# Optimization experiments

Hardware: AMD Instinct MI355X
Metric: run time of the kernel (lower is better)

## Reference

```python
import jax, jax.numpy as jnp
import numpy as np

B, S, T, E, H, Vt, Vs, M = 16, 64, 64, 256, 512, 32000, 32000, 100
J = 2 * M + 1


def _lstm(x, lengths, Wx, Wh, b, reverse=False):
    # TF LSTMCell (forget_bias=1.0) with sequence_length masking, optional reverse_sequence.
    Bn, Tn, _ = x.shape
    Hn = Wh.shape[0]
    tpos = jnp.arange(Tn)
    ridx = None
    if reverse:
        ridx = jnp.where(tpos[None, :] < lengths[:, None], lengths[:, None] - 1 - tpos[None, :], tpos[None, :])
        x = jnp.take_along_axis(x, ridx[:, :, None], axis=1)
    mask = (tpos[:, None] < lengths[None, :])[:, :, None]  # [T,B,1]
    xT = jnp.swapaxes(x, 0, 1)  # [T,B,E]

    def step(carry, inp):
        h, c = carry
        xt, mt = inp
        g = xt @ Wx + h @ Wh + b
        i, j, f, o = jnp.split(g, 4, axis=-1)
        c_new = jax.nn.sigmoid(f + 1.0) * c + jax.nn.sigmoid(i) * jnp.tanh(j)
        h_new = jax.nn.sigmoid(o) * jnp.tanh(c_new)
        c2 = jnp.where(mt, c_new, c)
        h2 = jnp.where(mt, h_new, h)
        return (h2, c2), jnp.where(mt, h_new, jnp.zeros_like(h_new))

    init = (jnp.zeros((Bn, Hn), x.dtype), jnp.zeros((Bn, Hn), x.dtype))
    _, ys = jax.lax.scan(step, init, (xT, mask))
    ys = jnp.swapaxes(ys, 0, 1)  # [B,T,H]
    if reverse:
        ys = jnp.take_along_axis(ys, ridx[:, :, None], axis=1)
    return ys


def setup_inputs() -> dict:
    key = jax.random.key(0)
    ks = jax.random.split(key, 24)
    sc = 0.05
    n = lambda k, shape: (jax.random.normal(k, shape, jnp.float32) * sc)
    inp = {
        "sources": jax.random.randint(ks[0], (B, S), 0, Vs, jnp.int32),
        "targets": jax.random.randint(ks[1], (B, T), 0, Vt, jnp.int32),
        "targets_null": jnp.array([Vt - 1], jnp.int32),
        "target_lengths": jax.random.randint(ks[2], (B,), T // 2, T + 1, jnp.int32),
        "emb": n(ks[3], (Vt, E)),
        "nnW": n(ks[4], (E, H)),
        "nnb": jnp.zeros((H,), jnp.float32),
        "Wx_fw": n(ks[5], (E, 4 * H)),
        "Wh_fw": n(ks[6], (H, 4 * H)),
        "b_fw": jnp.zeros((4 * H,), jnp.float32),
        "Wx_bw": n(ks[7], (E, 4 * H)),
        "Wh_bw": n(ks[8], (H, 4 * H)),
        "b_bw": jnp.zeros((4 * H,), jnp.float32),
        "Wproj_e": n(ks[9], (2 * H, H)),
        "Wv": n(ks[10], (H, Vs)),
        "bv": jnp.zeros((Vs,), jnp.float32),
        "Wproj_t": n(ks[11], (2 * H, E)),
        "Wj": n(ks[12], (H, J)),
        "bj": jnp.zeros((J,), jnp.float32),
        "Wp0": n(ks[13], (H, 1)),
        "bp0": jnp.zeros((1,), jnp.float32),
    }
    return inp


def reference(sources, targets, targets_null, target_lengths, emb, nnW, nnb,
              Wx_fw, Wh_fw, b_fw, Wx_bw, Wh_bw, b_bw, Wproj_e, Wv, bv,
              Wproj_t, Wj, bj, Wp0, bp0):
    x = emb[targets]                              # [B,T,E]
    x_null = emb[targets_null]                    # [1,E]
    null_state = jnp.tanh(x_null @ nnW + nnb)     # [1,H]
    h_fw = _lstm(x, target_lengths, Wx_fw, Wh_fw, b_fw, False)
    h_bw = _lstm(x, target_lengths, Wx_bw, Wh_bw, b_bw, True)
    h_cat = jnp.concatenate([h_fw, h_bw], axis=-1)  # [B,T,2H]

    # ---- emission ----
    ts = h_cat @ Wproj_e                          # [B,T,H]
    probs = jax.nn.softmax(ts @ Wv + bv, axis=-1)             # [B,T,Vs]
    null_probs = jax.nn.softmax(null_state @ Wv + bv, axis=-1)  # [1,Vs]
    e_word = jnp.take_along_axis(probs, sources[:, None, :].astype(jnp.int32), axis=2)  # [B,T,S]
    e_null = jnp.broadcast_to(null_probs[0][sources][:, None, :], e_word.shape)
    emission = jnp.concatenate([e_word, e_null], axis=1)       # [B,2T,S]

    # ---- transition ----
    tt = jnp.tanh((h_cat @ Wproj_t) @ nnW + nnb)  # [B,T,H]
    jump = jax.nn.softmax(tt @ Wj + bj, axis=-1)  # [B,T,J]
    p0 = jax.nn.sigmoid(tt @ Wp0 + bp0)[..., 0]   # [B,T]
    Tn = targets.shape[1]
    # entry (i,j) <- jump[i, M + j - i] (the tf.map_fn gather over word_idx)
    idx = M + jnp.arange(Tn)[None, :] - jnp.arange(Tn)[:, None]  # [T,T]
    jw = jnp.take_along_axis(jump, jnp.broadcast_to(idx[None], (jump.shape[0], Tn, Tn)), axis=2)  # [B,T,T]
    eye = jnp.eye(Tn, dtype=jw.dtype)
    half = jnp.concatenate([jw, p0[:, :, None] * eye], axis=2)            # [B,T,2T]
    transition = jnp.concatenate([half, half], axis=1)                    # [B,2T,2T]
    lhalf = jnp.concatenate([jnp.log(jw), jnp.log(p0)[:, :, None] * eye], axis=2)
    transition_log = jnp.concatenate([lhalf, lhalf], axis=1)
    return emission, transition, transition_log
```

## Files before the change

### kernel.cpp

```cpp
#include <hip/hip_runtime.h>
#include <hip/hip_bf16.h>
#include <math.h>

#define Bn 16
#define Sn 64
#define Tn 64
#define En 256
#define Hn 512
#define VS 32000
#define Jn 201
#define Mn 100

#define O_HCATF  0
#define O_DENOM  524288
#define O_NULLD  525312
#define O_SLOTS  525376
#define O_HBUF   527424
#define ZERO_N   560192
#define O_NS     560192
#define O_TS     560704
#define O_TSF    1084992
#define O_TTPRE  1347136
#define O_TTPF   1609280
#define O_TT     1740352
#define O_XF     2264640
#define O_WVC    2264640
#define O_WXFW   2395712
#define O_WXBW   2657856
#define O_WPEF   2920000
#define O_WPTF   3182144
#define O_NNWF   3313216
#define O_GX     3378752

typedef __attribute__((ext_vector_type(8))) short short8;
typedef __attribute__((ext_vector_type(4))) float f32x4;

__device__ __forceinline__ float sigf(float x) { return 1.0f / (1.0f + expf(-x)); }
__device__ __forceinline__ unsigned short tobf(float x) {
    __hip_bfloat16 h = __float2bfloat16(x);
    return *reinterpret_cast<unsigned short*>(&h);
}

__device__ __forceinline__ void dconvA(const float* __restrict__ A, uint4* __restrict__ out,
                                       int K, const int* __restrict__ gidx, int g) {
    int Kd = K >> 5;
    int lane = g & 63, t = g >> 6;
    int ks = t % Kd, mt = t / Kd;
    int m = mt * 16 + (lane & 15);
    int k0 = ks * 32 + (lane >> 4) * 8;
    const float* p = (gidx ? A + (size_t)gidx[m] * K : A + (size_t)m * K) + k0;
    float4 f0 = *(const float4*)(p);
    float4 f1 = *(const float4*)(p + 4);
    unsigned short u[8] = {tobf(f0.x), tobf(f0.y), tobf(f0.z), tobf(f0.w),
                           tobf(f1.x), tobf(f1.y), tobf(f1.z), tobf(f1.w)};
    out[g] = *(uint4*)u;
}

__device__ __forceinline__ void dconvB(const float* __restrict__ B, uint4* __restrict__ out,
                                       int N, int K, int g) {
    int Kd = K >> 5;
    int lane = g & 63, t = g >> 6;
    int ks = t % Kd, nt = t / Kd;
    int n = nt * 16 + (lane & 15);
    int k0 = ks * 32 + (lane >> 4) * 8;
    const float* p = B + (size_t)k0 * N + n;
    unsigned short u[8];
#pragma unroll
    for (int j = 0; j < 8; j++) u[j] = tobf(p[(size_t)j * N]);
    out[g] = *(uint4*)u;
}

__global__ __launch_bounds__(256) void convA2_k(const float* __restrict__ ttpre,
                                                uint4* __restrict__ ttpf,
                                                const float* __restrict__ ts,
                                                uint4* __restrict__ tsf) {
    int blk = blockIdx.x, tid = threadIdx.x;
    if (blk < 128) dconvA(ttpre, ttpf, 256, nullptr, blk * 256 + tid);
    else           dconvA(ts, tsf, 512, nullptr, (blk - 128) * 256 + tid);
}

__global__ __launch_bounds__(256) void mega_prep_k(float4* __restrict__ zdst, int zn4,
                                                   const float* __restrict__ emb,
                                                   const int* __restrict__ targets,
                                                   uint4* __restrict__ xf,
                                                   const float* __restrict__ wxfw, uint4* __restrict__ wxfwf,
                                                   const float* __restrict__ wxbw, uint4* __restrict__ wxbwf) {
    int blk = blockIdx.x, tid = threadIdx.x;
    if (blk < 548) {
        int i = blk * 256 + tid;
        if (i < zn4) zdst[i] = make_float4(0.f, 0.f, 0.f, 0.f);
    } else if (blk < 676) {
        dconvA(emb, xf, 256, targets, (blk - 548) * 256 + tid);
    } else if (blk < 932) {
        dconvB(wxfw, wxfwf, 2048, 256, (blk - 676) * 256 + tid);
    } else {
        dconvB(wxbw, wxbwf, 2048, 256, (blk - 932) * 256 + tid);
    }
}

template <int ACT>
__device__ __forceinline__ void gemm_body(const uint4* __restrict__ af,
                                          const uint4* __restrict__ bf,
                                          const float* __restrict__ bias,
                                          float* __restrict__ C, int N, int Kd,
                                          int bx, int by) {
    int tid = threadIdx.x, w = tid >> 6, lane = tid & 63;
    int ntb = bx * 8 + w * 2;
    int mtb = by * 8;
    f32x4 acc[8][2];
#pragma unroll
    for (int i = 0; i < 8; i++)
#pragma unroll
        for (int j = 0; j < 2; j++) acc[i][j] = 0.0f;
    for (int ks = 0; ks < Kd; ++ks) {
        uint4 b0 = bf[(size_t)(ntb * Kd + ks) * 64 + lane];
        uint4 b1 = bf[(size_t)((ntb + 1) * Kd + ks) * 64 + lane];
#pragma unroll
        for (int i = 0; i < 8; i++) {
            uint4 a = af[(size_t)((mtb + i) * Kd + ks) * 64 + lane];
            acc[i][0] = __builtin_amdgcn_mfma_f32_16x16x32_bf16(
                *reinterpret_cast<short8*>(&a), *reinterpret_cast<short8*>(&b0), acc[i][0], 0, 0, 0);
            acc[i][1] = __builtin_amdgcn_mfma_f32_16x16x32_bf16(
                *reinterpret_cast<short8*>(&a), *reinterpret_cast<short8*>(&b1), acc[i][1], 0, 0, 0);
        }
    }
    int n0 = ntb * 16 + (lane & 15);
    int q = lane >> 4;
    float bs0 = bias ? bias[n0] : 0.f;
    float bs1 = bias ? bias[n0 + 16] : 0.f;
#pragma unroll
    for (int i = 0; i < 8; i++)
#pragma unroll
        for (int r = 0; r < 4; r++) {
            int m = (mtb + i) * 16 + q * 4 + r;
            float v0 = acc[i][0][r] + bs0;
            float v1 = acc[i][1][r] + bs1;
            if (ACT == 1) { v0 = tanhf(v0); v1 = tanhf(v1); }
            C[(size_t)m * N + n0] = v0;
            C[(size_t)m * N + n0 + 16] = v1;
        }
}

template <int ACT>
__global__ __launch_bounds__(256) void gemm_mfma_k(const uint4* __restrict__ af,
                                                   const uint4* __restrict__ bf,
                                                   const float* __restrict__ bias,
                                                   float* __restrict__ C, int N, int Kd) {
    gemm_body<ACT>(af, bf, bias, C, N, Kd, blockIdx.x, blockIdx.y);
}

__global__ __launch_bounds__(256) void gx_gemm_k(const uint4* __restrict__ xf,
                                                 const uint4* __restrict__ wxfwf,
                                                 const uint4* __restrict__ wxbwf,
                                                 const float* __restrict__ b_fw,
                                                 const float* __restrict__ b_bw,
                                                 float* __restrict__ gx) {
    int bx = blockIdx.x;
    if (bx < 16) gemm_body<0>(xf, wxfwf, b_fw, gx, 2048, 8, bx, blockIdx.y);
    else         gemm_body<0>(xf, wxbwf, b_bw, gx + 2097152, 2048, 8, bx - 16, blockIdx.y);
}

__global__ __launch_bounds__(256) void proj_gemm_k(const uint4* __restrict__ hcatf,
                                                   const uint4* __restrict__ wpef,
                                                   const uint4* __restrict__ wptf,
                                                   float* __restrict__ ts,
                                                   float* __restrict__ ttpre) {
    int bx = blockIdx.x;
    if (bx < 4) gemm_body<0>(hcatf, wpef, nullptr, ts, 512, 32, bx, blockIdx.y);
    else        gemm_body<0>(hcatf, wptf, nullptr, ttpre, 256, 32, bx - 4, blockIdx.y);
}

__global__ __launch_bounds__(256, 1) void lstm_fused_k(const float* __restrict__ wh_fw,
                                                       const float* __restrict__ wh_bw,
                                                       const float* __restrict__ gx,
                                                       const int* __restrict__ lengths,
                                                       unsigned* __restrict__ hbuf32,
                                                       unsigned* __restrict__ hcat32,
                                                       unsigned* __restrict__ slots,
                                                       const float* __restrict__ Wv,
                                                       const float* __restrict__ emb,
                                                       const int* __restrict__ tnull,
                                                       const float* __restrict__ nnW,
                                                       const float* __restrict__ nnb,
                                                       const float* __restrict__ bv,
                                                       float* __restrict__ ns,
                                                       float* __restrict__ nd,
                                                       const int* __restrict__ sources,
                                                       float* __restrict__ wvc,
                                                       const float* __restrict__ wpe, uint4* __restrict__ wpef,
                                                       const float* __restrict__ wpt, uint4* __restrict__ wptf,
                                                       const float* __restrict__ nnw2, uint4* __restrict__ nnwf) {
    int blk = blockIdx.x;
    int tid = threadIdx.x;

    if (blk >= 669) {
        dconvB(nnw2, nnwf, 512, 256, (blk - 669) * 256 + tid);
        return;
    }
    if (blk >= 541) {
        dconvB(wpt, wptf, 256, 1024, (blk - 541) * 256 + tid);
        return;
    }
    if (blk >= 285) {
        dconvB(wpe, wpef, 512, 1024, (blk - 285) * 256 + tid);
        return;
    }
    if (blk >= 157) {
        int cb = blk - 157;
#pragma unroll
        for (int cc = 0; cc < 8; ++cc) {
            int ci = cb * 8 + cc;
            int c = sources[ci];
            float v0 = Wv[(size_t)tid * VS + c];
            float v1 = Wv[(size_t)(tid + 256) * VS + c];
            wvc[(size_t)ci * 512 + tid] = v0;
            wvc[(size_t)ci * 512 + 256 + tid] = v1;
        }
        return;
    }
    if (blk >= 32) {
        __shared__ float xn[En];
        __shared__ float nsl[Hn];
        __shared__ float red[4];
        int bid = blk - 32;
        xn[tid] = emb[(size_t)tnull[0] * En + tid];
        __syncthreads();
#pragma unroll
        for (int hh = 0; hh < 2; hh++) {
            int h = tid + hh * 256;
            float a = nnb[h];
            for (int e = 0; e < En; e++) a += xn[e] * nnW[(size_t)e * Hn + h];
            float v = tanhf(a);
            nsl[h] = v;
            if (bid == 0) ns[h] = v;
        }
        __syncthreads();
        int v = bid * 256 + tid;
        float a = bv[v];
        for (int k = 0; k < Hn; k++) a += nsl[k] * Wv[(size_t)k * VS + v];
        float e = expf(a);
        for (int o = 1; o < 64; o <<= 1) e += __shfl_xor(e, o);
        if ((tid & 63) == 0) red[tid >> 6] = e;
        __syncthreads();
        if (tid == 0) atomicAdd(nd, red[0] + red[1] + red[2] + red[3]);
        return;
    }

    __shared__ uint4 whf[8192];
    __shared__ float raw[32][129];
    __shared__ int lenS[16];
    int dir = blk >> 4;
    int u0 = (blk & 15) * 32;
    const float* wh = dir ? wh_bw : wh_fw;
    if (tid < 16) lenS[tid] = lengths[tid];

    for (int chunk = 0; chunk < 16; ++chunk) {
#pragma unroll
        for (int it = 0; it < 16; ++it) {
            int li = it * 256 + tid;
            int kl = li >> 7, c = li & 127;
            int g = c >> 5, ub = c & 31;
            raw[kl][c] = wh[(size_t)(chunk * 32 + kl) * 2048 + g * 512 + u0 + ub];
        }
        __syncthreads();
#pragma unroll
        for (int it = 0; it < 2; ++it) {
            int idx = tid * 2 + it;
            int w = idx >> 7, t = (idx >> 6) & 1, lane = idx & 63;
            int n = lane & 15, uu = n >> 1, p = n & 1;
            int cc = (t * 2 + p) * 32 + w * 8 + uu;
            int kb = (lane >> 4) * 8;
            unsigned short u8[8];
#pragma unroll
            for (int j = 0; j < 8; j++) u8[j] = tobf(raw[kb + j][cc]);
            whf[((w * 2 + t) * 16 + chunk) * 64 + lane] = *(uint4*)u8;
        }
        __syncthreads();
    }

    int wv = tid >> 6, lane = tid & 63;
    int n = lane & 15, uu = n >> 1, q = lane >> 4;
    int u = u0 + wv * 8 + uu;
    float creg[4] = {0.f, 0.f, 0.f, 0.f};
    unsigned short hbf[4] = {0, 0, 0, 0};

    for (int s = 0; s < 64; ++s) {
        float gxi[4], gxj[4], gxf[4], gxo[4];
#pragma unroll
        for (int r = 0; r < 4; r++) {
            int b = q * 4 + r;
            int len = lenS[b];
            int tc = dir ? (len - 1 - s) : s;
            tc = tc < 0 ? 0 : tc;
            const float* gp = gx + (size_t)dir * 2097152 + (size_t)(b * 64 + tc) * 2048 + u;
            gxi[r] = gp[0]; gxj[r] = gp[512]; gxf[r] = gp[1024]; gxo[r] = gp[1536];
        }
        const unsigned long long* hb64 =
            (const unsigned long long*)(hbuf32 + (((s & 1) * 2 + dir) * 16) * 256);
        unsigned long long h64[32];
#pragma unroll
        for (int ks = 0; ks < 16; ks++) {
            int idx = n * 128 + ks * 8 + q * 2;
            h64[2 * ks] = __hip_atomic_load(hb64 + idx, __ATOMIC_RELAXED, __HIP_MEMORY_SCOPE_AGENT);
            h64[2 * ks + 1] = __hip_atomic_load(hb64 + idx + 1, __ATOMIC_RELAXED, __HIP_MEMORY_SCOPE_AGENT);
        }
        f32x4 acc0 = {0.f, 0.f, 0.f, 0.f}, acc1 = {0.f, 0.f, 0.f, 0.f};
#pragma unroll
        for (int ks = 0; ks < 16; ks++) {
            unsigned long long av[2] = {h64[2 * ks], h64[2 * ks + 1]};
            short8 a = *reinterpret_cast<short8*>(av);
            uint4 b0 = whf[((wv * 2 + 0) * 16 + ks) * 64 + lane];
            uint4 b1 = whf[((wv * 2 + 1) * 16 + ks) * 64 + lane];
            acc0 = __builtin_amdgcn_mfma_f32_16x16x32_bf16(a, *reinterpret_cast<short8*>(&b0), acc0, 0, 0, 0);
            acc1 = __builtin_amdgcn_mfma_f32_16x16x32_bf16(a, *reinterpret_cast<short8*>(&b1), acc1, 0, 0, 0);
        }
#pragma unroll
        for (int r = 0; r < 4; r++) {
            float jvv = __shfl_xor(acc0[r], 1);
            float ovv = __shfl_xor(acc1[r], 1);
            int b = q * 4 + r;
            int len = lenS[b];
            float gi = acc0[r] + gxi[r];
            float gj = jvv + gxj[r];
            float gf = acc1[r] + gxf[r];
            float go = ovv + gxo[r];
            float cn = sigf(gf + 1.0f) * creg[r] + sigf(gi) * tanhf(gj);
            float hn = sigf(go) * tanhf(cn);
            if (s < len) { creg[r] = cn; hbf[r] = tobf(hn); }
        }
#pragma unroll
        for (int r = 0; r < 4; r++) {
            unsigned self = hbf[r];
            unsigned part = (unsigned)__shfl_xor((int)self, 2) & 0xffffu;
            if ((n & 3) == 0) {
                unsigned pk = self | (part << 16);
                int b = q * 4 + r;
                __hip_atomic_store(
                    hbuf32 + ((((s + 1) & 1) * 2 + dir) * 16 + b) * 256 + (u >> 1), pk,
                    __ATOMIC_RELAXED, __HIP_MEMORY_SCOPE_AGENT);
                int len = lenS[b];
                if (s < len) {
                    int tin = dir ? (len - 1 - s) : s;
                    int row = b * 64 + tin, col = dir * 512 + u;
                    int mt = row >> 4, ksx = col >> 5;
                    int lanep = (row & 15) | (((col >> 3) & 3) << 4);
                    hcat32[(size_t)(((mt * 32 + ksx) * 64 + lanep) * 4) + ((col & 7) >> 1)] = pk;
                }
            }
        }
        if (s == 63) break;
        __syncthreads();
        if (tid == 0)
            __hip_atomic_store(&slots[blk * 64], (unsigned)(s + 1), __ATOMIC_RELAXED,
                               __HIP_MEMORY_SCOPE_AGENT);
        if (tid < 16) {
            while (__hip_atomic_load(&slots[(dir * 16 + tid) * 64], __ATOMIC_RELAXED,
                                     __HIP_MEMORY_SCOPE_AGENT) < (unsigned)(s + 1)) {
                __builtin_amdgcn_s_sleep(1);
            }
        }
        __syncthreads();
    }
}

__global__ __launch_bounds__(256) void phaseA_mfma_k(const uint4* __restrict__ tsb,
                                                     const float* __restrict__ Wv,
                                                     const float* __restrict__ bv,
                                                     float* __restrict__ denom) {
    __shared__ uint4 wls[8192];
    __shared__ float redL[4][128];
    int tid = threadIdx.x;
    int wave = tid >> 6, lane = tid & 63;
    for (int it = 0; it < 32; ++it) {
        int g = it * 256 + tid;
        int gl = g & 63, t = g >> 6;
        int ks = t & 15, tl = t >> 4;
        int nt = blockIdx.x * 8 + tl;
        int nn = nt * 16 + (gl & 15);
        int k0 = ks * 32 + (gl >> 4) * 8;
        const float* p = Wv + (size_t)k0 * VS + nn;
        unsigned short u[8];
#pragma unroll
        for (int j = 0; j < 8; j++) u[j] = tobf(p[(size_t)j * VS]);
        wls[g] = *(uint4*)u;
    }
    __syncthreads();

    int ntbase = blockIdx.x * 8 + wave * 2;
    float bv0 = bv[ntbase * 16 + (lane & 15)];
    float bv1 = bv[(ntbase + 1) * 16 + (lane & 15)];
    int q = lane >> 4;
    for (int mc = 0; mc < 8; ++mc) {
        f32x4 acc[8][2];
#pragma unroll
        for (int i = 0; i < 8; i++)
#pragma unroll
            for (int j = 0; j < 2; j++) acc[i][j] = 0.0f;
#pragma unroll 4
        for (int ks = 0; ks < 16; ++ks) {
            short8 a[8], b[2];
#pragma unroll
            for (int i = 0; i < 8; i++) {
                int mt = mc * 8 + i;
                uint4 t = tsb[(size_t)(mt * 16 + ks) * 64 + lane];
                a[i] = *reinterpret_cast<short8*>(&t);
            }
#pragma unroll
            for (int j = 0; j < 2; j++) {
                uint4 t = wls[((wave * 2 + j) * 16 + ks) * 64 + lane];
                b[j] = *reinterpret_cast<short8*>(&t);
            }
#pragma unroll
            for (int i = 0; i < 8; i++)
#pragma unroll
                for (int j = 0; j < 2; j++)
                    acc[i][j] = __builtin_amdgcn_mfma_f32_16x16x32_bf16(a[i], b[j], acc[i][j], 0, 0, 0);
        }
#pragma unroll
        for (int i = 0; i < 8; i++) {
#pragma unroll
            for (int r = 0; r < 4; r++) {
                float e = __expf(acc[i][0][r] + bv0) + __expf(acc[i][1][r] + bv1);
                e += __shfl_xor(e, 1);
                e += __shfl_xor(e, 2);
                e += __shfl_xor(e, 4);
                e += __shfl_xor(e, 8);
                if ((lane & 15) == 0) redL[wave][i * 16 + q * 4 + r] = e;
            }
        }
        __syncthreads();
        if (tid < 128) {
            float v = redL[0][tid] + redL[1][tid] + redL[2][tid] + redL[3][tid];
            atomicAdd(&denom[mc * 128 + tid], v);
        }
        __syncthreads();
    }
}

__global__ __launch_bounds__(512) void emission_k(const float* __restrict__ ts,
                                                  const float* __restrict__ wvc,
                                                  const float* __restrict__ bv,
                                                  const int* __restrict__ sources,
                                                  const float* __restrict__ ns,
                                                  const float* __restrict__ denom,
                                                  const float* __restrict__ nulld,
                                                  float* __restrict__ em) {
    __shared__ float colv[512];
    __shared__ float red[64][9];
    __shared__ float red2[8];
    __shared__ float env_s, bvc_s;
    int b = blockIdx.y, sc = blockIdx.x;
    int tid = threadIdx.x;
    for (int qq = 0; qq < 8; ++qq) {
        int s = sc * 8 + qq;
        int ci = b * 64 + s;
        __syncthreads();
        colv[tid] = wvc[(size_t)ci * 512 + tid];
        if (tid == 0) bvc_s = bv[sources[ci]];
        __syncthreads();
        int r = tid & 63, ksl = tid >> 6;
        const float* tr = ts + (size_t)(b * 64 + r) * 512 + ksl * 64;
        float p = 0.f;
#pragma unroll
        for (int k4 = 0; k4 < 16; k4++) {
            float4 t4 = *(const float4*)(tr + k4 * 4);
            float4 c4 = *(const float4*)&colv[ksl * 64 + k4 * 4];
            p += t4.x * c4.x + t4.y * c4.y + t4.z * c4.z + t4.w * c4.w;
        }
        red[r][ksl] = p;
        if (tid < 8) {
            float pn = 0.f;
#pragma unroll
            for (int k4 = 0; k4 < 16; k4++) {
                float4 n4 = *(const float4*)(ns + tid * 64 + k4 * 4);
                float4 c4 = *(const float4*)&colv[tid * 64 + k4 * 4];
                pn += n4.x * c4.x + n4.y * c4.y + n4.z * c4.z + n4.w * c4.w;
            }
            red2[tid] = pn;
        }
        __syncthreads();
        if (tid < 64) {
            float dot = red[tid][0] + red[tid][1] + red[tid][2] + red[tid][3] +
                        red[tid][4] + red[tid][5] + red[tid][6] + red[tid][7];
            float ew = expf(dot + bvc_s) / denom[b * 64 + tid];
            em[(size_t)(b * 128 + tid) * 64 + s] = ew;
        } else if (tid == 64) {
            float dn = red2[0] + red2[1] + red2[2] + red2[3] +
                       red2[4] + red2[5] + red2[6] + red2[7];
            env_s = expf(dn + bvc_s) / nulld[0];
        }
        __syncthreads();
        if (tid < 64) em[(size_t)(b * 128 + 64 + tid) * 64 + s] = env_s;
    }
}

__global__ __launch_bounds__(256) void transition_k(const float* __restrict__ tt,
                                                    const float* __restrict__ Wj,
                                                    const float* __restrict__ bj,
                                                    const float* __restrict__ Wp0,
                                                    const float* __restrict__ bp0,
                                                    float* __restrict__ trans,
                                                    float* __restrict__ tlog) {
    __shared__ float ttl[512];
    __shared__ float jrow[Jn], ljrow[Jn];
    __shared__ float sred[256];
    __shared__ float p0_s, lp0_s;
    int blk = blockIdx.x;
    int b = blk >> 6, i = blk & 63;
    int tid = threadIdx.x;
    {
        const float* trr = tt + (size_t)blk * 512;
        if (tid < 128) *(float4*)&ttl[tid * 4] = *(const float4*)(trr + tid * 4);
    }
    __syncthreads();
    bool isj = tid < Jn;
    bool isp = tid == Jn;
    float l = 0.f;
    if (isj || isp) {
        const float* wb = isj ? (Wj + tid) : Wp0;
        int stride = isj ? Jn : 1;
        float a = isj ? bj[tid] : bp0[0];
        for (int k = 0; k < 512; k++) a += ttl[k] * wb[(size_t)k * stride];
        l = a;
    }
    sred[tid] = isj ? l : -1e30f;
    __syncthreads();
    for (int o = 128; o > 0; o >>= 1) {
        if (tid < o) sred[tid] = fmaxf(sred[tid], sred[tid + o]);
        __syncthreads();
    }
    float m = sred[0];
    __syncthreads();
    float ex = isj ? expf(l - m) : 0.f;
    sred[tid] = ex;
    __syncthreads();
    for (int o = 128; o > 0; o >>= 1) {
        if (tid < o) sred[tid] += sred[tid + o];
        __syncthreads();
    }
    float S = sred[0];
    if (isj) {
        jrow[tid] = ex / S;
        ljrow[tid] = (l - m) - logf(S);
    }
    if (isp) {
        float pv = 1.f / (1.f + expf(-l));
        p0_s = pv;
        lp0_s = logf(pv);
    }
    __syncthreads();
    if (tid < 128) {
        int j = tid;
        float tv, lv;
        if (j < 64) {
            int id = Mn + j - i;
            tv = jrow[id];
            lv = ljrow[id];
        } else {
            bool dg = (j - 64) == i;
            tv = dg ? p0_s : 0.f;
            lv = dg ? lp0_s : 0.f;
        }
        size_t r1 = (size_t)(b * 128 + i) * 128 + j;
        size_t r2 = (size_t)(b * 128 + 64 + i) * 128 + j;
        trans[r1] = tv;
        trans[r2] = tv;
        tlog[r1] = lv;
        tlog[r2] = lv;
    }
}

extern "C" void kernel_launch(void* const* d_in, const int* in_sizes, int n_in,
                              void* d_out, int out_size, void* d_ws, size_t ws_size,
                              hipStream_t stream) {
    const int* sources = (const int*)d_in[0];
    const int* targets = (const int*)d_in[1];
    const int* tnull = (const int*)d_in[2];
    const int* lengths = (const int*)d_in[3];
    const float* emb = (const float*)d_in[4];
    const float* nnW = (const float*)d_in[5];
    const float* nnb = (const float*)d_in[6];
    const float* Wx_fw = (const float*)d_in[7];
    const float* Wh_fw = (const float*)d_in[8];
    const float* b_fw = (const float*)d_in[9];
    const float* Wx_bw = (const float*)d_in[10];
    const float* Wh_bw = (const float*)d_in[11];
    const float* b_bw = (const float*)d_in[12];
    const float* Wproj_e = (const float*)d_in[13];
    const float* Wv = (const float*)d_in[14];
    const float* bv = (const float*)d_in[15];
    const float* Wproj_t = (const float*)d_in[16];
    const float* Wj = (const float*)d_in[17];
    const float* bj = (const float*)d_in[18];
    const float* Wp0 = (const float*)d_in[19];
    const float* bp0 = (const float*)d_in[20];

    float* ws = (float*)d_ws;
    float* out = (float*)d_out;
    float* out_em = out;
    float* out_tr = out + 131072;
    float* out_tl = out + 131072 + 262144;

    mega_prep_k<<<1188, 256, 0, stream>>>((float4*)ws, ZERO_N / 4,
                                          emb, targets, (uint4*)(ws + O_XF),
                                          Wx_fw, (uint4*)(ws + O_WXFW),
                                          Wx_bw, (uint4*)(ws + O_WXBW));

    gx_gemm_k<<<dim3(32, 8), 256, 0, stream>>>((uint4*)(ws + O_XF), (uint4*)(ws + O_WXFW),
                                               (uint4*)(ws + O_WXBW), b_fw, b_bw, ws + O_GX);

    lstm_fused_k<<<733, 256, 0, stream>>>(Wh_fw, Wh_bw, ws + O_GX, lengths,
                                          (unsigned*)(ws + O_HBUF), (unsigned*)(ws + O_HCATF),
                                          (unsigned*)(ws + O_SLOTS),
                                          Wv, emb, tnull, nnW, nnb, bv,
                                          ws + O_NS, ws + O_NULLD,
                                          sources, ws + O_WVC,
                                          Wproj_e, (uint4*)(ws + O_WPEF),
                                          Wproj_t, (uint4*)(ws + O_WPTF),
                                          nnW, (uint4*)(ws + O_NNWF));

    proj_gemm_k<<<dim3(6, 8), 256, 0, stream>>>((uint4*)(ws + O_HCATF), (uint4*)(ws + O_WPEF),
                                                (uint4*)(ws + O_WPTF), ws + O_TS, ws + O_TTPRE);

    convA2_k<<<384, 256, 0, stream>>>(ws + O_TTPRE, (uint4*)(ws + O_TTPF),
                                      ws + O_TS, (uint4*)(ws + O_TSF));
    gemm_mfma_k<1><<<dim3(4, 8), 256, 0, stream>>>((uint4*)(ws + O_TTPF), (uint4*)(ws + O_NNWF),
                                                   nnb, ws + O_TT, 512, 8);

    phaseA_mfma_k<<<250, 256, 0, stream>>>((const uint4*)(ws + O_TSF),
                                           Wv, bv, ws + O_DENOM);

    emission_k<<<dim3(8, 16), 512, 0, stream>>>(ws + O_TS, ws + O_WVC, bv, sources, ws + O_NS,
                                                ws + O_DENOM, ws + O_NULLD, out_em);

    transition_k<<<1024, 256, 0, stream>>>(ws + O_TT, Wj, bj, Wp0, bp0, out_tr, out_tl);
}
```

Before: 872.3 us.

## Precombine Wproj_t with nnW and merge transition into phase-A kernel

Computes the weight product Wproj_t @ nnW once, early in the gx GEMM kernel, so the transition hidden state becomes a single GEMM with tanh fused into the projection kernel. This removes the separate intermediate projection, its bf16 conversion and a follow-up GEMM launch. The transition kernel is also merged into the denominator (phase A) kernel as extra blocks, so they run concurrently and the chain has fewer launches. Rounding the combined weight to bf16 changes numerics slightly.

```diff
diff --git a/kernel.cpp b/kernel.cpp
--- a/kernel.cpp
+++ b/kernel.cpp
@@ -19,16 +19,16 @@
 #define ZERO_N   560192
 #define O_NS     560192
 #define O_TS     560704
+#define O_WCOMB  560704
 #define O_TSF    1084992
-#define O_TTPRE  1347136
-#define O_TTPF   1609280
+#define O_WCOMBF 1347136
+#define O_WPTAF  1609280
 #define O_TT     1740352
 #define O_XF     2264640
 #define O_WVC    2264640
 #define O_WXFW   2395712
 #define O_WXBW   2657856
 #define O_WPEF   2920000
-#define O_WPTF   3182144
 #define O_NNWF   3313216
 #define O_GX     3378752
 
@@ -70,13 +70,10 @@
     out[g] = *(uint4*)u;
 }
 
-__global__ __launch_bounds__(256) void convA2_k(const float* __restrict__ ttpre,
-                                                uint4* __restrict__ ttpf,
-                                                const float* __restrict__ ts,
-                                                uint4* __restrict__ tsf) {
-    int blk = blockIdx.x, tid = threadIdx.x;
-    if (blk < 128) dconvA(ttpre, ttpf, 256, nullptr, blk * 256 + tid);
-    else           dconvA(ts, tsf, 512, nullptr, (blk - 128) * 256 + tid);
+__global__ __launch_bounds__(256) void convA_k(const float* __restrict__ A,
+                                               uint4* __restrict__ out, int K,
+                                               const int* __restrict__ gidx) {
+    dconvA(A, out, K, gidx, blockIdx.x * 256 + threadIdx.x);
 }
 
 __global__ __launch_bounds__(256) void mega_prep_k(float4* __restrict__ zdst, int zn4,
@@ -84,7 +81,9 @@
                                                    const int* __restrict__ targets,
                                                    uint4* __restrict__ xf,
                                                    const float* __restrict__ wxfw, uint4* __restrict__ wxfwf,
-                                                   const float* __restrict__ wxbw, uint4* __restrict__ wxbwf) {
+                                                   const float* __restrict__ wxbw, uint4* __restrict__ wxbwf,
+                                                   const float* __restrict__ wpt, uint4* __restrict__ wptaf,
+                                                   const float* __restrict__ nnw, uint4* __restrict__ nnwf) {
     int blk = blockIdx.x, tid = threadIdx.x;
     if (blk < 548) {
         int i = blk * 256 + tid;
@@ -93,8 +92,12 @@
         dconvA(emb, xf, 256, targets, (blk - 548) * 256 + tid);
     } else if (blk < 932) {
         dconvB(wxfw, wxfwf, 2048, 256, (blk - 676) * 256 + tid);
+    } else if (blk < 1188) {
+        dconvB(wxbw, wxbwf, 2048, 256, (blk - 932) * 256 + tid);
+    } else if (blk < 1316) {
+        dconvA(wpt, wptaf, 256, nullptr, (blk - 1188) * 256 + tid);
     } else {
-        dconvB(wxbw, wxbwf, 2048, 256, (blk - 932) * 256 + tid);
+        dconvB(nnw, nnwf, 512, 256, (blk - 1316) * 256 + tid);
     }
 }
 
@@ -141,33 +144,30 @@
         }
 }
 
-template <int ACT>
-__global__ __launch_bounds__(256) void gemm_mfma_k(const uint4* __restrict__ af,
-                                                   const uint4* __restrict__ bf,
-                                                   const float* __restrict__ bias,
-                                                   float* __restrict__ C, int N, int Kd) {
-    gemm_body<ACT>(af, bf, bias, C, N, Kd, blockIdx.x, blockIdx.y);
-}
-
-__global__ __launch_bounds__(256) void gx_gemm_k(const uint4* __restrict__ xf,
-                                                 const uint4* __restrict__ wxfwf,
-                                                 const uint4* __restrict__ wxbwf,
-                                                 const float* __restrict__ b_fw,
-                                                 const float* __restrict__ b_bw,
-                                                 float* __restrict__ gx) {
+__global__ __launch_bounds__(256) void gxw_gemm_k(const uint4* __restrict__ xf,
+                                                  const uint4* __restrict__ wxfwf,
+                                                  const uint4* __restrict__ wxbwf,
+                                                  const float* __restrict__ b_fw,
+                                                  const float* __restrict__ b_bw,
+                                                  float* __restrict__ gx,
+                                                  const uint4* __restrict__ wptaf,
+                                                  const uint4* __restrict__ nnwf,
+                                                  float* __restrict__ wcomb) {
     int bx = blockIdx.x;
-    if (bx < 16) gemm_body<0>(xf, wxfwf, b_fw, gx, 2048, 8, bx, blockIdx.y);
-    else         gemm_body<0>(xf, wxbwf, b_bw, gx + 2097152, 2048, 8, bx - 16, blockIdx.y);
-}
-
-__global__ __launch_bounds__(256) void proj_gemm_k(const uint4* __restrict__ hcatf,
-                                                   const uint4* __restrict__ wpef,
-                                                   const uint4* __restrict__ wptf,
-                                                   float* __restrict__ ts,
-                                                   float* __restrict__ ttpre) {
+    if (bx < 16)      gemm_body<0>(xf, wxfwf, b_fw, gx, 2048, 8, bx, blockIdx.y);
+    else if (bx < 32) gemm_body<0>(xf, wxbwf, b_bw, gx + 2097152, 2048, 8, bx - 16, blockIdx.y);
+    else              gemm_body<0>(wptaf, nnwf, nullptr, wcomb, 512, 8, bx - 32, blockIdx.y);
+}
+
+__global__ __launch_bounds__(256) void projts_k(const uint4* __restrict__ hcatf,
+                                                const uint4* __restrict__ wpef,
+                                                const uint4* __restrict__ wcombf,
+                                                const float* __restrict__ nnb,
+                                                float* __restrict__ ts,
+                                                float* __restrict__ tt) {
     int bx = blockIdx.x;
     if (bx < 4) gemm_body<0>(hcatf, wpef, nullptr, ts, 512, 32, bx, blockIdx.y);
-    else        gemm_body<0>(hcatf, wptf, nullptr, ttpre, 256, 32, bx - 4, blockIdx.y);
+    else        gemm_body<1>(hcatf, wcombf, nnb, tt, 512, 32, bx - 4, blockIdx.y);
 }
 
 __global__ __launch_bounds__(256, 1) void lstm_fused_k(const float* __restrict__ wh_fw,
@@ -188,17 +188,12 @@
                                                        const int* __restrict__ sources,
                                                        float* __restrict__ wvc,
                                                        const float* __restrict__ wpe, uint4* __restrict__ wpef,
-                                                       const float* __restrict__ wpt, uint4* __restrict__ wptf,
-                                                       const float* __restrict__ nnw2, uint4* __restrict__ nnwf) {
+                                                       const float* __restrict__ wcomb, uint4* __restrict__ wcombf) {
     int blk = blockIdx.x;
     int tid = threadIdx.x;
 
-    if (blk >= 669) {
-        dconvB(nnw2, nnwf, 512, 256, (blk - 669) * 256 + tid);
-        return;
-    }
     if (blk >= 541) {
-        dconvB(wpt, wptf, 256, 1024, (blk - 541) * 256 + tid);
+        dconvB(wcomb, wcombf, 512, 1024, (blk - 541) * 256 + tid);
         return;
     }
     if (blk >= 285) {
@@ -363,77 +358,156 @@
     }
 }
 
-__global__ __launch_bounds__(256) void phaseA_mfma_k(const uint4* __restrict__ tsb,
-                                                     const float* __restrict__ Wv,
-                                                     const float* __restrict__ bv,
-                                                     float* __restrict__ denom) {
+__global__ __launch_bounds__(256) void phtr_k(const uint4* __restrict__ tsb,
+                                              const float* __restrict__ Wv,
+                                              const float* __restrict__ bv,
+                                              float* __restrict__ denom,
+                                              const float* __restrict__ tt,
+                                              const float* __restrict__ Wj,
+                                              const float* __restrict__ bj,
+                                              const float* __restrict__ Wp0,
+                                              const float* __restrict__ bp0,
+                                              float* __restrict__ trans,
+                                              float* __restrict__ tlog) {
     __shared__ uint4 wls[8192];
     __shared__ float redL[4][128];
+    __shared__ float ttl[512];
+    __shared__ float jrow[Jn], ljrow[Jn];
+    __shared__ float sred[256];
+    __shared__ float p0_s, lp0_s;
+    int blk = blockIdx.x;
     int tid = threadIdx.x;
-    int wave = tid >> 6, lane = tid & 63;
-    for (int it = 0; it < 32; ++it) {
-        int g = it * 256 + tid;
-        int gl = g & 63, t = g >> 6;
-        int ks = t & 15, tl = t >> 4;
-        int nt = blockIdx.x * 8 + tl;
-        int nn = nt * 16 + (gl & 15);
-        int k0 = ks * 32 + (gl >> 4) * 8;
-        const float* p = Wv + (size_t)k0 * VS + nn;
-        unsigned short u[8];
-#pragma unroll
-        for (int j = 0; j < 8; j++) u[j] = tobf(p[(size_t)j * VS]);
-        wls[g] = *(uint4*)u;
+
+    if (blk < 250) {
+        int wave = tid >> 6, lane = tid & 63;
+        for (int it = 0; it < 32; ++it) {
+            int g = it * 256 + tid;
+            int gl = g & 63, t = g >> 6;
+            int ks = t & 15, tl = t >> 4;
+            int nt = blk * 8 + tl;
+            int nn = nt * 16 + (gl & 15);
+            int k0 = ks * 32 + (gl >> 4) * 8;
+            const float* p = Wv + (size_t)k0 * VS + nn;
+            unsigned short u[8];
+#pragma unroll
+            for (int j = 0; j < 8; j++) u[j] = tobf(p[(size_t)j * VS]);
+            wls[g] = *(uint4*)u;
+        }
+        __syncthreads();
+
+        int ntbase = blk * 8 + wave * 2;
+        float bv0 = bv[ntbase * 16 + (lane & 15)];
+        float bv1 = bv[(ntbase + 1) * 16 + (lane & 15)];
+        int q = lane >> 4;
+        for (int mc = 0; mc < 8; ++mc) {
+            f32x4 acc[8][2];
+#pragma unroll
+            for (int i = 0; i < 8; i++)
+#pragma unroll
+                for (int j = 0; j < 2; j++) acc[i][j] = 0.0f;
+#pragma unroll 4
+            for (int ks = 0; ks < 16; ++ks) {
+                short8 a[8], b[2];
+#pragma unroll
+                for (int i = 0; i < 8; i++) {
+                    int mt = mc * 8 + i;
+                    uint4 t = tsb[(size_t)(mt * 16 + ks) * 64 + lane];
+                    a[i] = *reinterpret_cast<short8*>(&t);
+                }
+#pragma unroll
+                for (int j = 0; j < 2; j++) {
+                    uint4 t = wls[((wave * 2 + j) * 16 + ks) * 64 + lane];
+                    b[j] = *reinterpret_cast<short8*>(&t);
+                }
+#pragma unroll
+                for (int i = 0; i < 8; i++)
+#pragma unroll
+                    for (int j = 0; j < 2; j++)
+                        acc[i][j] = __builtin_amdgcn_mfma_f32_16x16x32_bf16(a[i], b[j], acc[i][j], 0, 0, 0);
+            }
+#pragma unroll
+            for (int i = 0; i < 8; i++) {
+#pragma unroll
+                for (int r = 0; r < 4; r++) {
+                    float e = __expf(acc[i][0][r] + bv0) + __expf(acc[i][1][r] + bv1);
+                    e += __shfl_xor(e, 1);
+                    e += __shfl_xor(e, 2);
+                    e += __shfl_xor(e, 4);
+                    e += __shfl_xor(e, 8);
+                    if ((lane & 15) == 0) redL[wave][i * 16 + q * 4 + r] = e;
+                }
+            }
+            __syncthreads();
+            if (tid < 128) {
+                float v = redL[0][tid] + redL[1][tid] + redL[2][tid] + redL[3][tid];
+                atomicAdd(&denom[mc * 128 + tid], v);
+            }
+            __syncthreads();
+        }
+        return;
+    }
+
+    int tb = blk - 250;
+    int b = tb >> 6, i = tb & 63;
+    {
+        const float* trr = tt + (size_t)tb * 512;
+        if (tid < 128) *(float4*)&ttl[tid * 4] = *(const float4*)(trr + tid * 4);
     }
     __syncthreads();
-
-    int ntbase = blockIdx.x * 8 + wave * 2;
-    float bv0 = bv[ntbase * 16 + (lane & 15)];
-    float bv1 = bv[(ntbase + 1) * 16 + (lane & 15)];
-    int q = lane >> 4;
-    for (int mc = 0; mc < 8; ++mc) {
-        f32x4 acc[8][2];
-#pragma unroll
-        for (int i = 0; i < 8; i++)
-#pragma unroll
-            for (int j = 0; j < 2; j++) acc[i][j] = 0.0f;
-#pragma unroll 4
-        for (int ks = 0; ks < 16; ++ks) {
-            short8 a[8], b[2];
-#pragma unroll
-            for (int i = 0; i < 8; i++) {
-                int mt = mc * 8 + i;
-                uint4 t = tsb[(size_t)(mt * 16 + ks) * 64 + lane];
-                a[i] = *reinterpret_cast<short8*>(&t);
-            }
-#pragma unroll
-            for (int j = 0; j < 2; j++) {
-                uint4 t = wls[((wave * 2 + j) * 16 + ks) * 64 + lane];
-                b[j] = *reinterpret_cast<short8*>(&t);
-            }
-#pragma unroll
-            for (int i = 0; i < 8; i++)
-#pragma unroll
-                for (int j = 0; j < 2; j++)
-                    acc[i][j] = __builtin_amdgcn_mfma_f32_16x16x32_bf16(a[i], b[j], acc[i][j], 0, 0, 0);
-        }
-#pragma unroll
-        for (int i = 0; i < 8; i++) {
-#pragma unroll
-            for (int r = 0; r < 4; r++) {
-                float e = __expf(acc[i][0][r] + bv0) + __expf(acc[i][1][r] + bv1);
-                e += __shfl_xor(e, 1);
-                e += __shfl_xor(e, 2);
-                e += __shfl_xor(e, 4);
-                e += __shfl_xor(e, 8);
-                if ((lane & 15) == 0) redL[wave][i * 16 + q * 4 + r] = e;
-            }
-        }
-        __syncthreads();
-        if (tid < 128) {
-            float v = redL[0][tid] + redL[1][tid] + redL[2][tid] + redL[3][tid];
-            atomicAdd(&denom[mc * 128 + tid], v);
-        }
-        __syncthreads();
+    bool isj = tid < Jn;
+    bool isp = tid == Jn;
+    float l = 0.f;
+    if (isj || isp) {
+        const float* wb = isj ? (Wj + tid) : Wp0;
+        int stride = isj ? Jn : 1;
+        float a = isj ? bj[tid] : bp0[0];
+        for (int k = 0; k < 512; k++) a += ttl[k] * wb[(size_t)k * stride];
+        l = a;
+    }
+    sred[tid] = isj ? l : -1e30f;
+    __syncthreads();
+    for (int o = 128; o > 0; o >>= 1) {
+        if (tid < o) sred[tid] = fmaxf(sred[tid], sred[tid + o]);
+        __syncthreads();
+    }
+    float m = sred[0];
+    __syncthreads();
+    float ex = isj ? expf(l - m) : 0.f;
+    sred[tid] = ex;
+    __syncthreads();
+    for (int o = 128; o > 0; o >>= 1) {
+        if (tid < o) sred[tid] += sred[tid + o];
+        __syncthreads();
+    }
+    float S = sred[0];
+    if (isj) {
+        jrow[tid] = ex / S;
+        ljrow[tid] = (l - m) - logf(S);
+    }
+    if (isp) {
+        float pv = 1.f / (1.f + expf(-l));
+        p0_s = pv;
+        lp0_s = logf(pv);
+    }
+    __syncthreads();
+    if (tid < 128) {
+        int j = tid;
+        float tv, lv;
+        if (j < 64) {
+            int id = Mn + j - i;
+            tv = jrow[id];
+            lv = ljrow[id];
+        } else {
+            bool dg = (j - 64) == i;
+            tv = dg ? p0_s : 0.f;
+            lv = dg ? lp0_s : 0.f;
+        }
+        size_t r1 = (size_t)(b * 128 + i) * 128 + j;
+        size_t r2 = (size_t)(b * 128 + 64 + i) * 128 + j;
+        trans[r1] = tv;
+        trans[r2] = tv;
+        tlog[r1] = lv;
+        tlog[r2] = lv;
     }
 }
 
@@ -491,82 +565,6 @@
         }
         __syncthreads();
         if (tid < 64) em[(size_t)(b * 128 + 64 + tid) * 64 + s] = env_s;
-    }
-}
-
-__global__ __launch_bounds__(256) void transition_k(const float* __restrict__ tt,
-                                                    const float* __restrict__ Wj,
-                                                    const float* __restrict__ bj,
-                                                    const float* __restrict__ Wp0,
-                                                    const float* __restrict__ bp0,
-                                                    float* __restrict__ trans,
-                                                    float* __restrict__ tlog) {
-    __shared__ float ttl[512];
-    __shared__ float jrow[Jn], ljrow[Jn];
-    __shared__ float sred[256];
-    __shared__ float p0_s, lp0_s;
-    int blk = blockIdx.x;
-    int b = blk >> 6, i = blk & 63;
-    int tid = threadIdx.x;
-    {
-        const float* trr = tt + (size_t)blk * 512;
-        if (tid < 128) *(float4*)&ttl[tid * 4] = *(const float4*)(trr + tid * 4);
-    }
-    __syncthreads();
-    bool isj = tid < Jn;
-    bool isp = tid == Jn;
-    float l = 0.f;
-    if (isj || isp) {
-        const float* wb = isj ? (Wj + tid) : Wp0;
-        int stride = isj ? Jn : 1;
-        float a = isj ? bj[tid] : bp0[0];
-        for (int k = 0; k < 512; k++) a += ttl[k] * wb[(size_t)k * stride];
-        l = a;
-    }
-    sred[tid] = isj ? l : -1e30f;
-    __syncthreads();
-    for (int o = 128; o > 0; o >>= 1) {
-        if (tid < o) sred[tid] = fmaxf(sred[tid], sred[tid + o]);
-        __syncthreads();
-    }
-    float m = sred[0];
-    __syncthreads();
-    float ex = isj ? expf(l - m) : 0.f;
-    sred[tid] = ex;
-    __syncthreads();
-    for (int o = 128; o > 0; o >>= 1) {
-        if (tid < o) sred[tid] += sred[tid + o];
-        __syncthreads();
-    }
-    float S = sred[0];
-    if (isj) {
-        jrow[tid] = ex / S;
-        ljrow[tid] = (l - m) - logf(S);
-    }
-    if (isp) {
-        float pv = 1.f / (1.f + expf(-l));
-        p0_s = pv;
-        lp0_s = logf(pv);
-    }
-    __syncthreads();
-    if (tid < 128) {
-        int j = tid;
-        float tv, lv;
-        if (j < 64) {
-            int id = Mn + j - i;
-            tv = jrow[id];
-            lv = ljrow[id];
-        } else {
-            bool dg = (j - 64) == i;
-            tv = dg ? p0_s : 0.f;
-            lv = dg ? lp0_s : 0.f;
-        }
-        size_t r1 = (size_t)(b * 128 + i) * 128 + j;
-        size_t r2 = (size_t)(b * 128 + 64 + i) * 128 + j;
-        trans[r1] = tv;
-        trans[r2] = tv;
-        tlog[r1] = lv;
-        tlog[r2] = lv;
     }
 }
 
@@ -601,37 +599,36 @@
     float* out_tr = out + 131072;
     float* out_tl = out + 131072 + 262144;
 
-    mega_prep_k<<<1188, 256, 0, stream>>>((float4*)ws, ZERO_N / 4,
+    mega_prep_k<<<1380, 256, 0, stream>>>((float4*)ws, ZERO_N / 4,
                                           emb, targets, (uint4*)(ws + O_XF),
                                           Wx_fw, (uint4*)(ws + O_WXFW),
-                                          Wx_bw, (uint4*)(ws + O_WXBW));
-
-    gx_gemm_k<<<dim3(32, 8), 256, 0, stream>>>((uint4*)(ws + O_XF), (uint4*)(ws + O_WXFW),
-                                               (uint4*)(ws + O_WXBW), b_fw, b_bw, ws + O_GX);
-
-    lstm_fused_k<<<733, 256, 0, stream>>>(Wh_fw, Wh_bw, ws + O_GX, lengths,
+                                          Wx_bw, (uint4*)(ws + O_WXBW),
+                                          Wproj_t, (uint4*)(ws + O_WPTAF),
+                                          nnW, (uint4*)(ws + O_NNWF));
+
+    gxw_gemm_k<<<dim3(36, 8), 256, 0, stream>>>((uint4*)(ws + O_XF), (uint4*)(ws + O_WXFW),
+                                                (uint4*)(ws + O_WXBW), b_fw, b_bw, ws + O_GX,
+                                                (uint4*)(ws + O_WPTAF), (uint4*)(ws + O_NNWF),
+                                                ws + O_WCOMB);
+
+    lstm_fused_k<<<797, 256, 0, stream>>>(Wh_fw, Wh_bw, ws + O_GX, lengths,
                                           (unsigned*)(ws + O_HBUF), (unsigned*)(ws + O_HCATF),
                                           (unsigned*)(ws + O_SLOTS),
                                           Wv, emb, tnull, nnW, nnb, bv,
                                           ws + O_NS, ws + O_NULLD,
                                           sources, ws + O_WVC,
                                           Wproj_e, (uint4*)(ws + O_WPEF),
-                                          Wproj_t, (uint4*)(ws + O_WPTF),
-                                          nnW, (uint4*)(ws + O_NNWF));
-
-    proj_gemm_k<<<dim3(6, 8), 256, 0, stream>>>((uint4*)(ws + O_HCATF), (uint4*)(ws + O_WPEF),
-                                                (uint4*)(ws + O_WPTF), ws + O_TS, ws + O_TTPRE);
-
-    convA2_k<<<384, 256, 0, stream>>>(ws + O_TTPRE, (uint4*)(ws + O_TTPF),
-                                      ws + O_TS, (uint4*)(ws + O_TSF));
-    gemm_mfma_k<1><<<dim3(4, 8), 256, 0, stream>>>((uint4*)(ws + O_TTPF), (uint4*)(ws + O_NNWF),
-                                                   nnb, ws + O_TT, 512, 8);
-
-    phaseA_mfma_k<<<250, 256, 0, stream>>>((const uint4*)(ws + O_TSF),
-                                           Wv, bv, ws + O_DENOM);
+                                          ws + O_WCOMB, (uint4*)(ws + O_WCOMBF));
+
+    projts_k<<<dim3(8, 8), 256, 0, stream>>>((uint4*)(ws + O_HCATF), (uint4*)(ws + O_WPEF),
+                                             (uint4*)(ws + O_WCOMBF), nnb,
+                                             ws + O_TS, ws + O_TT);
+
+    convA_k<<<256, 256, 0, stream>>>(ws + O_TS, (uint4*)(ws + O_TSF), 512, nullptr);
+
+    phtr_k<<<1274, 256, 0, stream>>>((const uint4*)(ws + O_TSF), Wv, bv, ws + O_DENOM,
+                                     ws + O_TT, Wj, bj, Wp0, bp0, out_tr, out_tl);
 
     emission_k<<<dim3(8, 16), 512, 0, stream>>>(ws + O_TS, ws + O_WVC, bv, sources, ws + O_NS,
                                                 ws + O_DENOM, ws + O_NULLD, out_em);
-
-    transition_k<<<1024, 256, 0, stream>>>(ws + O_TT, Wj, bj, Wp0, bp0, out_tr, out_tl);
-}
+}
```

Result: slower. 929.1 us (+6.5%).
